# Performance work log

Hardware: AMD Instinct MI355X
Metric: run time of the kernel (lower is better)

Reference implementation:

```python
import jax, jax.numpy as jnp
import numpy as np

D_MODEL = 1024
NUM_HEADS = 16
D_K = D_MODEL // NUM_HEADS


def setup_inputs() -> dict:
    key = jax.random.key(0)
    ks = jax.random.split(key, 5)
    sd = np.sqrt(2.0 / (D_MODEL + D_MODEL))
    x = jax.random.normal(ks[0], (2, 2048, D_MODEL), dtype=jnp.float32)
    # weights stored as [out_features, in_features] like torch Linear
    w_q = jax.random.normal(ks[1], (D_MODEL, D_MODEL), dtype=jnp.float32) * (sd * sd)
    w_k = jax.random.normal(ks[2], (D_MODEL, D_MODEL), dtype=jnp.float32) * (sd * sd)
    w_v = jax.random.normal(ks[3], (D_MODEL, D_MODEL), dtype=jnp.float32) * (sd * sd)
    w_o = jax.random.normal(ks[4], (D_MODEL, D_MODEL), dtype=jnp.float32) * (sd * sd)
    return {"x": x, "w_q": w_q, "w_k": w_k, "w_v": w_v, "w_o": w_o}


def reference(x, w_q, w_k, w_v, w_o):
    B, S, D = x.shape
    H, Dk = NUM_HEADS, D_K
    # projections: x @ W.T
    q = (x @ w_q.T).reshape(B, S, H, Dk).transpose(0, 2, 1, 3)  # [B,H,S,Dk]
    k = (x @ w_k.T).reshape(B, S, H, Dk).transpose(0, 2, 1, 3)
    v = (x @ w_v.T).reshape(B, S, H, Dk).transpose(0, 2, 1, 3)
    scale = 1.0 / np.sqrt(Dk).astype(np.float32)
    scores = jnp.einsum('bhqd,bhkd->bhqk', q, k) * scale  # [B,H,S,S]
    causal = jnp.tril(jnp.ones((S, S), dtype=bool))
    scores = jnp.where(causal, scores, -jnp.inf)
    weights = jax.nn.softmax(scores, axis=-1)
    attn = jnp.einsum('bhqk,bhkd->bhqd', weights, v)  # [B,H,S,Dk]
    attn = attn.transpose(0, 2, 1, 3).reshape(B, S, D)
    return attn @ w_o.T
```

## Files before the change

### kernel.cpp

```cpp
#include <hip/hip_runtime.h>

typedef __attribute__((ext_vector_type(8))) short short8;
typedef __attribute__((ext_vector_type(4))) float f32x4;
typedef __attribute__((ext_vector_type(16))) float f32x16;
typedef __attribute__((ext_vector_type(2))) unsigned int u32x2;

#define DM 1024
#define SL 2048
#define NH 16
#define DKH 64
#define NB 2

__device__ __forceinline__ unsigned short f2bf(float f) {
    union { float f; unsigned int u; } a; a.f = f;
    unsigned int r = a.u + 0x7FFFu + ((a.u >> 16) & 1u);
    return (unsigned short)(r >> 16);
}

__device__ __forceinline__ void gl_lds16(const void* g, void* l) {
    __builtin_amdgcn_global_load_lds(
        (__attribute__((address_space(1))) void*)(g),
        (__attribute__((address_space(3))) void*)(l), 16, 0, 0);
}

__device__ __forceinline__ unsigned int cvtpk_bf16(float lo, float hi) {
    unsigned int r;
    asm("v_cvt_pk_bf16_f32 %0, %1, %2" : "=v"(r) : "v"(lo), "v"(hi));
    return r;
}

__device__ __forceinline__ void pl32swap(unsigned int &a, unsigned int &b) {
    u32x2 r = __builtin_amdgcn_permlane32_swap(a, b, false, false);
    a = r[0]; b = r[1];
}
__device__ __forceinline__ void pl32swapf(float &a, float &b) {
    unsigned int ua = __float_as_uint(a), ub = __float_as_uint(b);
    pl32swap(ua, ub);
    a = __uint_as_float(ua); b = __uint_as_float(ub);
}

__global__ __launch_bounds__(256) void convert_kernel(
    const float* __restrict__ x,  const float* __restrict__ wq,
    const float* __restrict__ wk, const float* __restrict__ wv,
    const float* __restrict__ wo,
    unsigned short* __restrict__ xb,  unsigned short* __restrict__ wqb,
    unsigned short* __restrict__ wkb, unsigned short* __restrict__ wvb,
    unsigned short* __restrict__ wob)
{
    const int NX = NB * SL * DM;
    const int NW = DM * DM;
    int t4 = (blockIdx.x * 256 + threadIdx.x) * 4;
    const float* src; unsigned short* dst; int off; float scale = 1.0f;
    if (t4 < NX)              { src = x;  dst = xb;  off = t4; }
    else if (t4 < NX + NW)    { src = wq; dst = wqb; off = t4 - NX; scale = 0.125f * 1.44269504088896f; }
    else if (t4 < NX + 2*NW)  { src = wk; dst = wkb; off = t4 - NX - NW; }
    else if (t4 < NX + 3*NW)  { src = wv; dst = wvb; off = t4 - NX - 2*NW; }
    else                      { src = wo; dst = wob; off = t4 - NX - 3*NW; }
    float4 v = *(const float4*)(src + off);
    unsigned long long p =
        (unsigned long long)f2bf(v.x * scale)
      | ((unsigned long long)f2bf(v.y * scale) << 16)
      | ((unsigned long long)f2bf(v.z * scale) << 32)
      | ((unsigned long long)f2bf(v.w * scale) << 48);
    *(unsigned long long*)(dst + off) = p;
}

__global__ __launch_bounds__(256) void gemm_bt(
    const unsigned short* __restrict__ A,
    const unsigned short* __restrict__ Bw,
    unsigned short* __restrict__ oq, unsigned short* __restrict__ ok,
    unsigned short* __restrict__ ov)
{
    __shared__ __align__(16) unsigned short As[128 * 64];
    __shared__ __align__(16) unsigned short Bs[128 * 64];
    const int tid  = threadIdx.x;
    const int lane = tid & 63;
    const int wave = tid >> 6;
    const int wm = (wave >> 1) * 64, wn = (wave & 1) * 64;
    const int bx = blockIdx.x, by = blockIdx.y;
    const int c    = lane & 15;
    const int kg16 = (lane >> 4) * 16;
    const int swz  = (c & 7) << 4;

    f32x4 acc[4][4];
    #pragma unroll
    for (int i = 0; i < 4; i++)
        #pragma unroll
        for (int j = 0; j < 4; j++) acc[i][j] = (f32x4){0.f, 0.f, 0.f, 0.f};

    const char* Ab = (const char*)A  + by * 128 * (DM * 2);
    const char* Bb = (const char*)Bw + bx * 128 * (DM * 2);

    for (int k0 = 0; k0 < DM; k0 += 64) {
        #pragma unroll
        for (int i = 0; i < 4; i++) {
            int o  = i * 4096 + tid * 16;
            int r  = o >> 7;
            int cb = o & 127;
            int src = r * (DM * 2) + k0 * 2 + (cb ^ ((r & 7) << 4));
            gl_lds16(Ab + src, (char*)As + o);
            gl_lds16(Bb + src, (char*)Bs + o);
        }
        __syncthreads();
        #pragma unroll
        for (int kk = 0; kk < 2; kk++) {
            short8 a[4], bfr[4];
            #pragma unroll
            for (int mi = 0; mi < 4; mi++)
                a[mi] = *(const short8*)((const char*)As
                        + (wm + mi * 16 + c) * 128 + ((kk * 64 + kg16) ^ swz));
            #pragma unroll
            for (int ni = 0; ni < 4; ni++)
                bfr[ni] = *(const short8*)((const char*)Bs
                        + (wn + ni * 16 + c) * 128 + ((kk * 64 + kg16) ^ swz));
            #pragma unroll
            for (int mi = 0; mi < 4; mi++)
                #pragma unroll
                for (int ni = 0; ni < 4; ni++)
                    acc[mi][ni] = __builtin_amdgcn_mfma_f32_16x16x32_bf16(
                        a[mi], bfr[ni], acc[mi][ni], 0, 0, 0);
        }
        __syncthreads();
    }

    const int r4 = (lane >> 4) * 4;
    const int mat = (bx * 128) >> 10;
    unsigned short* outb = (mat == 0) ? oq : (mat == 1) ? ok : ov;
    const int nb = bx * 128 - (mat << 10);
    #pragma unroll
    for (int mi = 0; mi < 4; mi++) {
        int m_g = by * 128 + wm + mi * 16 + r4;
        int b_  = m_g >> 11, s_ = m_g & 2047;
        #pragma unroll
        for (int ni = 0; ni < 4; ni++) {
            int n_l = nb + wn + ni * 16 + c;
            int h = n_l >> 6, dk = n_l & 63;
            #pragma unroll
            for (int j = 0; j < 4; j++)
                outb[((b_ * NH + h) * SL + (s_ + j)) * DKH + dk] = f2bf(acc[mi][ni][j]);
        }
    }
}

__global__ __launch_bounds__(256) void gemm_o(
    const unsigned short* __restrict__ A,
    const unsigned short* __restrict__ Bw,
    float* __restrict__ of)
{
    __shared__ __align__(16) unsigned short As[64 * 64];
    __shared__ __align__(16) unsigned short Bs[128 * 64];
    const int tid  = threadIdx.x;
    const int lane = tid & 63;
    const int wave = tid >> 6;
    const int wm = (wave >> 1) * 32, wn = (wave & 1) * 64;
    const int bx = blockIdx.x, by = blockIdx.y;
    const int c    = lane & 15;
    const int kg16 = (lane >> 4) * 16;
    const int swz  = (c & 7) << 4;

    f32x4 acc[2][4];
    #pragma unroll
    for (int i = 0; i < 2; i++)
        #pragma unroll
        for (int j = 0; j < 4; j++) acc[i][j] = (f32x4){0.f, 0.f, 0.f, 0.f};

    const char* Ab = (const char*)A  + by * 64  * (DM * 2);
    const char* Bb = (const char*)Bw + bx * 128 * (DM * 2);

    for (int k0 = 0; k0 < DM; k0 += 64) {
        #pragma unroll
        for (int i = 0; i < 2; i++) {
            int o  = i * 4096 + tid * 16;
            int r  = o >> 7, cb = o & 127;
            int src = r * (DM * 2) + k0 * 2 + (cb ^ ((r & 7) << 4));
            gl_lds16(Ab + src, (char*)As + o);
        }
        #pragma unroll
        for (int i = 0; i < 4; i++) {
            int o  = i * 4096 + tid * 16;
            int r  = o >> 7, cb = o & 127;
            int src = r * (DM * 2) + k0 * 2 + (cb ^ ((r & 7) << 4));
            gl_lds16(Bb + src, (char*)Bs + o);
        }
        __syncthreads();
        #pragma unroll
        for (int kk = 0; kk < 2; kk++) {
            short8 a[2], bfr[4];
            #pragma unroll
            for (int mi = 0; mi < 2; mi++)
                a[mi] = *(const short8*)((const char*)As
                        + (wm + mi * 16 + c) * 128 + ((kk * 64 + kg16) ^ swz));
            #pragma unroll
            for (int ni = 0; ni < 4; ni++)
                bfr[ni] = *(const short8*)((const char*)Bs
                        + (wn + ni * 16 + c) * 128 + ((kk * 64 + kg16) ^ swz));
            #pragma unroll
            for (int mi = 0; mi < 2; mi++)
                #pragma unroll
                for (int ni = 0; ni < 4; ni++)
                    acc[mi][ni] = __builtin_amdgcn_mfma_f32_16x16x32_bf16(
                        a[mi], bfr[ni], acc[mi][ni], 0, 0, 0);
        }
        __syncthreads();
    }

    const int r4 = (lane >> 4) * 4;
    #pragma unroll
    for (int mi = 0; mi < 2; mi++) {
        int m_g = by * 64 + wm + mi * 16 + r4;
        #pragma unroll
        for (int ni = 0; ni < 4; ni++) {
            int n_g = bx * 128 + wn + ni * 16 + c;
            #pragma unroll
            for (int j = 0; j < 4; j++)
                of[(m_g + j) * DM + n_g] = acc[mi][ni][j];
        }
    }
}

__global__ __launch_bounds__(128) void attn_kernel(
    const unsigned short* __restrict__ Q,
    const unsigned short* __restrict__ K,
    const unsigned short* __restrict__ V,
    unsigned short* __restrict__ O,
    unsigned short* __restrict__ partO,
    float* __restrict__ ml)
{
    __shared__ __align__(16) unsigned short Kl[2][64 * 64];
    __shared__ __align__(16) unsigned short Vt[2][8 * 64 * 8];
    const int tid = threadIdx.x, lane = tid & 63, wave = tid >> 6;
    const int ln31 = lane & 31, hi = lane >> 5;
    const int item = blockIdx.x >> 5;
    const int bh   = blockIdx.x & 31;
    int qt, cch, t0, ntc;
    if (item < 16)      { qt = 16 + item;              cch = 0; t0 = 0;  ntc = 16; }
    else if (item < 32) { int j = item - 16; qt = 31 - j; cch = 1; t0 = 16; ntc = 16 - j; }
    else                { int j = item - 32; qt = 15 - j; cch = 0; t0 = 0;  ntc = 16 - j; }
    const int b = bh >> 4, h = bh & 15;
    const int bhi = b * NH + h;
    const unsigned short* Qg = Q + bhi * (SL * DKH);
    const unsigned short* Kg = K + bhi * (SL * DKH);
    const unsigned short* Vg = V + bhi * (SL * DKH);
    const int qw = qt * 64 + wave * 32;
    const int vd0 = (tid & 31) * 2, c0 = tid >> 5;

    short8 qf[4];
    #pragma unroll
    for (int ks = 0; ks < 4; ks++)
        qf[ks] = *(const short8*)&Qg[(qw + ln31) * DKH + ks * 16 + hi * 8];

    f32x16 OT0, OT1;
    #pragma unroll
    for (int r = 0; r < 16; r++) { OT0[r] = 0.f; OT1[r] = 0.f; }
    float mrun = -1e30f, ls = 0.f;

    unsigned int vreg[16];

    {
        const size_t kvb = (size_t)t0 * 64;
        #pragma unroll
        for (int i = 0; i < 4; i++) {
            int s = i * 128 + tid;
            int kv = s >> 3;
            int k8 = (s & 7) ^ (kv & 7);
            gl_lds16((const char*)Kg + (kvb + kv) * 128 + k8 * 16,
                     (char*)&Kl[0][0] + s * 16);
        }
        #pragma unroll
        for (int c2 = 0; c2 < 2; c2++)
            #pragma unroll
            for (int i = 0; i < 8; i++)
                vreg[c2 * 8 + i] = *(const unsigned int*)&Vg[(kvb + (c0 + 4 * c2) * 8 + i) * DKH + vd0];
    }

    for (int tt = 0; tt < ntc; ++tt) {
        const int t = t0 + tt;
        const int buf = tt & 1;
        const int kv0 = t * 64;
        #pragma unroll
        for (int c2 = 0; c2 < 2; c2++) {
            int chunk = c0 + 4 * c2;
            short8 sa, sb;
            #pragma unroll
            for (int i = 0; i < 8; i++) {
                unsigned int pr = vreg[c2 * 8 + i];
                sa[i] = (short)(pr & 0xFFFFu);
                sb[i] = (short)(pr >> 16);
            }
            *(short8*)&Vt[buf][(chunk * 64 + vd0) * 8]     = sa;
            *(short8*)&Vt[buf][(chunk * 64 + vd0 + 1) * 8] = sb;
        }
        __syncthreads();

        if (tt + 1 < ntc) {
            const size_t kv1 = (size_t)(t + 1) * 64;
            #pragma unroll
            for (int i = 0; i < 4; i++) {
                int s = i * 128 + tid;
                int kv = s >> 3;
                int k8 = (s & 7) ^ (kv & 7);
                gl_lds16((const char*)Kg + (kv1 + kv) * 128 + k8 * 16,
                         (char*)&Kl[buf ^ 1][0] + s * 16);
            }
            #pragma unroll
            for (int c2 = 0; c2 < 2; c2++)
                #pragma unroll
                for (int i = 0; i < 8; i++)
                    vreg[c2 * 8 + i] = *(const unsigned int*)&Vg[(kv1 + (c0 + 4 * c2) * 8 + i) * DKH + vd0];
        }

        const char* kb = (const char*)&Kl[buf][0];
        const unsigned short* vb = &Vt[buf][0];

        f32x16 S0, S1;
        #pragma unroll
        for (int r = 0; r < 16; r++) { S0[r] = 0.f; S1[r] = 0.f; }
        __builtin_amdgcn_s_setprio(1);
        #pragma unroll
        for (int ks = 0; ks < 4; ks++) {
            int ko = (ks * 32 + hi * 16) ^ ((ln31 & 7) << 4);
            short8 ka0 = *(const short8*)(kb + ln31 * 128 + ko);
            short8 ka1 = *(const short8*)(kb + (32 + ln31) * 128 + ko);
            S0 = __builtin_amdgcn_mfma_f32_32x32x16_bf16(ka0, qf[ks], S0, 0, 0, 0);
            S1 = __builtin_amdgcn_mfma_f32_32x32x16_bf16(ka1, qf[ks], S1, 0, 0, 0);
        }
        __builtin_amdgcn_s_setprio(0);

        if (t == qt) {
            const int qrel0 = qw + ln31 - kv0 - 4 * hi;
            const int qrel1 = qrel0 - 32;
            #pragma unroll
            for (int r = 0; r < 16; r++) {
                const int ro = (r & 3) + 8 * (r >> 2);
                if (ro > qrel0) S0[r] = -1e30f;
                if (ro > qrel1) S1[r] = -1e30f;
            }
        }

        float mx = fmaxf(S0[0], S1[0]);
        #pragma unroll
        for (int r = 1; r < 16; r++) mx = fmaxf(mx, fmaxf(S0[r], S1[r]));
        float ma = mx, mb = mx;
        pl32swapf(ma, mb);
        float rm = fmaxf(ma, mb);

        if (__any(rm > mrun + 8.f)) {
            float nm = fmaxf(mrun, rm);
            float corr = __builtin_amdgcn_exp2f(mrun - nm);
            mrun = nm; ls *= corr;
            #pragma unroll
            for (int r = 0; r < 16; r++) { OT0[r] *= corr; OT1[r] *= corr; }
        }

        float psum = 0.f;
        #pragma unroll
        for (int r = 0; r < 16; r++) {
            S0[r] = __builtin_amdgcn_exp2f(S0[r] - mrun); psum += S0[r];
            S1[r] = __builtin_amdgcn_exp2f(S1[r] - mrun); psum += S1[r];
        }
        ls += psum;

        short8 pf[4];
        {
            unsigned int wa, wb, wc, wd;
            wa = cvtpk_bf16(S0[0], S0[1]);   wb = cvtpk_bf16(S0[4], S0[5]);
            pl32swap(wa, wb);
            wc = cvtpk_bf16(S0[2], S0[3]);   wd = cvtpk_bf16(S0[6], S0[7]);
            pl32swap(wc, wd);
            union { unsigned int u[4]; short8 s; } w0 = {{wa, wc, wb, wd}};
            pf[0] = w0.s;

            wa = cvtpk_bf16(S0[8], S0[9]);   wb = cvtpk_bf16(S0[12], S0[13]);
            pl32swap(wa, wb);
            wc = cvtpk_bf16(S0[10], S0[11]); wd = cvtpk_bf16(S0[14], S0[15]);
            pl32swap(wc, wd);
            union { unsigned int u[4]; short8 s; } w1 = {{wa, wc, wb, wd}};
            pf[1] = w1.s;

            wa = cvtpk_bf16(S1[0], S1[1]);   wb = cvtpk_bf16(S1[4], S1[5]);
            pl32swap(wa, wb);
            wc = cvtpk_bf16(S1[2], S1[3]);   wd = cvtpk_bf16(S1[6], S1[7]);
            pl32swap(wc, wd);
            union { unsigned int u[4]; short8 s; } w2 = {{wa, wc, wb, wd}};
            pf[2] = w2.s;

            wa = cvtpk_bf16(S1[8], S1[9]);   wb = cvtpk_bf16(S1[12], S1[13]);
            pl32swap(wa, wb);
            wc = cvtpk_bf16(S1[10], S1[11]); wd = cvtpk_bf16(S1[14], S1[15]);
            pl32swap(wc, wd);
            union { unsigned int u[4]; short8 s; } w3 = {{wa, wc, wb, wd}};
            pf[3] = w3.s;
        }

        __builtin_amdgcn_s_setprio(1);
        #pragma unroll
        for (int ks2 = 0; ks2 < 4; ks2++) {
            int slot = (ks2 * 2 + hi) * 64;
            short8 va0 = *(const short8*)&vb[(slot + ln31) * 8];
            short8 va1 = *(const short8*)&vb[(slot + 32 + ln31) * 8];
            OT0 = __builtin_amdgcn_mfma_f32_32x32x16_bf16(va0, pf[ks2], OT0, 0, 0, 0);
            OT1 = __builtin_amdgcn_mfma_f32_32x32x16_bf16(va1, pf[ks2], OT1, 0, 0, 0);
        }
        __builtin_amdgcn_s_setprio(0);
    }

    float la = ls, lb = ls;
    pl32swapf(la, lb);
    const float lrow = la + lb;
    const int qrow_l = wave * 32 + ln31;
    if (qt >= 16) {
        const int rec = (bh * 16 + (qt - 16)) * 2 + cch;
        unsigned short* po = partO + (size_t)rec * 4096;
        if (hi == 0) {
            ml[(rec * 64 + qrow_l) * 2]     = mrun;
            ml[(rec * 64 + qrow_l) * 2 + 1] = lrow;
        }
        #pragma unroll
        for (int r = 0; r < 16; r++) {
            const int d0 = (r & 3) + 8 * (r >> 2) + 4 * hi;
            po[qrow_l * 64 + d0]      = f2bf(OT0[r]);
            po[qrow_l * 64 + 32 + d0] = f2bf(OT1[r]);
        }
    } else {
        float inv = 1.0f / lrow;
        const int qrow = qw + ln31;
        const size_t base = (size_t)(b * SL + qrow) * DM + h * DKH;
        #pragma unroll
        for (int r = 0; r < 16; r++) {
            const int d0 = (r & 3) + 8 * (r >> 2) + 4 * hi;
            O[base + d0]      = f2bf(OT0[r] * inv);
            O[base + 32 + d0] = f2bf(OT1[r] * inv);
        }
    }
}

__global__ __launch_bounds__(256) void combine_kernel(
    const unsigned short* __restrict__ partO,
    const float* __restrict__ ml,
    unsigned short* __restrict__ O)
{
    const int gi = blockIdx.x * 8 + (threadIdx.x >> 5);
    const int ln = threadIdx.x & 31;
    const int bh = gi >> 10, rem = gi & 1023;
    const int qtl = rem >> 6, row = rem & 63;
    const int qt = 16 + qtl;
    const int rec0 = (bh * 16 + qtl) * 2;
    const float m0 = ml[(rec0 * 64 + row) * 2];
    const float l0 = ml[(rec0 * 64 + row) * 2 + 1];
    const float m1 = ml[((rec0 + 1) * 64 + row) * 2];
    const float l1 = ml[((rec0 + 1) * 64 + row) * 2 + 1];
    const float M  = fmaxf(m0, m1);
    const float w0 = exp2f(m0 - M), w1 = exp2f(m1 - M);
    const float inv = 1.0f / (w0 * l0 + w1 * l1);
    const unsigned int u0 = *(const unsigned int*)&partO[(size_t)rec0 * 4096 + row * 64 + ln * 2];
    const unsigned int u1 = *(const unsigned int*)&partO[(size_t)(rec0 + 1) * 4096 + row * 64 + ln * 2];
    const float a0 = __uint_as_float(u0 << 16);
    const float b0 = __uint_as_float(u0 & 0xFFFF0000u);
    const float a1 = __uint_as_float(u1 << 16);
    const float b1 = __uint_as_float(u1 & 0xFFFF0000u);
    const float oa = (a0 * w0 + a1 * w1) * inv;
    const float ob = (b0 * w0 + b1 * w1) * inv;
    const unsigned int pack = (unsigned int)f2bf(oa) | ((unsigned int)f2bf(ob) << 16);
    const int b = bh >> 4, h = bh & 15;
    const size_t base = (size_t)(b * SL + qt * 64 + row) * DM + h * DKH;
    *(unsigned int*)&O[base + ln * 2] = pack;
}

extern "C" void kernel_launch(void* const* d_in, const int* in_sizes, int n_in,
                              void* d_out, int out_size, void* d_ws, size_t ws_size,
                              hipStream_t stream)
{
    const float* x  = (const float*)d_in[0];
    const float* wq = (const float*)d_in[1];
    const float* wk = (const float*)d_in[2];
    const float* wv = (const float*)d_in[3];
    const float* wo = (const float*)d_in[4];
    char* ws = (char*)d_ws;
    unsigned short* xb  = (unsigned short*)(ws);
    unsigned short* wqb = (unsigned short*)(ws + (8ll  << 20));
    unsigned short* wkb = (unsigned short*)(ws + (10ll << 20));
    unsigned short* wvb = (unsigned short*)(ws + (12ll << 20));
    unsigned short* wob = (unsigned short*)(ws + (14ll << 20));
    unsigned short* Qb  = (unsigned short*)(ws + (16ll << 20));
    unsigned short* Kb  = (unsigned short*)(ws + (24ll << 20));
    unsigned short* Vb  = (unsigned short*)(ws + (32ll << 20));
    unsigned short* Abf = (unsigned short*)(ws + (40ll << 20));
    unsigned short* partO = (unsigned short*)(ws);
    float*          mlbuf = (float*)(ws + (8ll << 20));
    float* out = (float*)d_out;

    convert_kernel<<<dim3(8192), dim3(256), 0, stream>>>(
        x, wq, wk, wv, wo, xb, wqb, wkb, wvb, wob);

    gemm_bt<<<dim3(24, 32), dim3(256), 0, stream>>>(xb, wqb, Qb, Kb, Vb);

    attn_kernel<<<dim3(1536), dim3(128), 0, stream>>>(Qb, Kb, Vb, Abf, partO, mlbuf);
    combine_kernel<<<dim3(4096), dim3(256), 0, stream>>>(partO, mlbuf, Abf);

    gemm_o<<<dim3(8, 64), dim3(256), 0, stream>>>(Abf, wob, out);
}
```

Before: 104.8 us.

## Use 128-row query tiles with four waves sharing each K/V tile

The attention kernel now runs 256-thread blocks covering 128 query rows (four waves), so each K/V tile staged in LDS serves twice as many queries. The work split is rebuilt: query tiles 8-15 are split into two KV chunks that are merged by the combine kernel, and tiles 0-7 run unsplit. Waves whose rows lie entirely before a KV tile skip its compute but still join the barriers. The aim is to halve K/V global and LDS staging traffic per query. In exchange there are half as many blocks, more causal-mask waste on diagonal tiles, and some waves sit idle, which may hurt load balance.

```diff
diff --git a/kernel.cpp b/kernel.cpp
--- a/kernel.cpp
+++ b/kernel.cpp
@@ -218,7 +218,7 @@
     }
 }
 
-__global__ __launch_bounds__(128) void attn_kernel(
+__global__ __launch_bounds__(256) void attn_kernel(
     const unsigned short* __restrict__ Q,
     const unsigned short* __restrict__ K,
     const unsigned short* __restrict__ V,
@@ -230,18 +230,17 @@
     __shared__ __align__(16) unsigned short Vt[2][8 * 64 * 8];
     const int tid = threadIdx.x, lane = tid & 63, wave = tid >> 6;
     const int ln31 = lane & 31, hi = lane >> 5;
-    const int item = blockIdx.x >> 5;
-    const int bh   = blockIdx.x & 31;
-    int qt, cch, t0, ntc;
-    if (item < 16)      { qt = 16 + item;              cch = 0; t0 = 0;  ntc = 16; }
-    else if (item < 32) { int j = item - 16; qt = 31 - j; cch = 1; t0 = 16; ntc = 16 - j; }
-    else                { int j = item - 32; qt = 15 - j; cch = 0; t0 = 0;  ntc = 16 - j; }
+    const int w  = blockIdx.x >> 5;
+    const int bh = blockIdx.x & 31;
+    int p, cch, t0, ntc;
+    if (w < 16) { p = 15 - (w >> 1); cch = w & 1; ntc = p + 1; t0 = cch ? (p + 1) : 0; }
+    else        { p = 23 - w; cch = 0; t0 = 0; ntc = 2 * p + 2; }
     const int b = bh >> 4, h = bh & 15;
     const int bhi = b * NH + h;
     const unsigned short* Qg = Q + bhi * (SL * DKH);
     const unsigned short* Kg = K + bhi * (SL * DKH);
     const unsigned short* Vg = V + bhi * (SL * DKH);
-    const int qw = qt * 64 + wave * 32;
+    const int qw = p * 128 + wave * 32;
     const int vd0 = (tid & 31) * 2, c0 = tid >> 5;
 
     short8 qf[4];
@@ -254,60 +253,56 @@
     for (int r = 0; r < 16; r++) { OT0[r] = 0.f; OT1[r] = 0.f; }
     float mrun = -1e30f, ls = 0.f;
 
-    unsigned int vreg[16];
+    unsigned int vreg[8];
 
     {
         const size_t kvb = (size_t)t0 * 64;
         #pragma unroll
-        for (int i = 0; i < 4; i++) {
-            int s = i * 128 + tid;
+        for (int i = 0; i < 2; i++) {
+            int s = i * 256 + tid;
             int kv = s >> 3;
             int k8 = (s & 7) ^ (kv & 7);
             gl_lds16((const char*)Kg + (kvb + kv) * 128 + k8 * 16,
                      (char*)&Kl[0][0] + s * 16);
         }
         #pragma unroll
-        for (int c2 = 0; c2 < 2; c2++)
-            #pragma unroll
-            for (int i = 0; i < 8; i++)
-                vreg[c2 * 8 + i] = *(const unsigned int*)&Vg[(kvb + (c0 + 4 * c2) * 8 + i) * DKH + vd0];
+        for (int i = 0; i < 8; i++)
+            vreg[i] = *(const unsigned int*)&Vg[(kvb + c0 * 8 + i) * DKH + vd0];
     }
 
     for (int tt = 0; tt < ntc; ++tt) {
         const int t = t0 + tt;
         const int buf = tt & 1;
         const int kv0 = t * 64;
-        #pragma unroll
-        for (int c2 = 0; c2 < 2; c2++) {
-            int chunk = c0 + 4 * c2;
+        {
             short8 sa, sb;
             #pragma unroll
             for (int i = 0; i < 8; i++) {
-                unsigned int pr = vreg[c2 * 8 + i];
+                unsigned int pr = vreg[i];
                 sa[i] = (short)(pr & 0xFFFFu);
                 sb[i] = (short)(pr >> 16);
             }
-            *(short8*)&Vt[buf][(chunk * 64 + vd0) * 8]     = sa;
-            *(short8*)&Vt[buf][(chunk * 64 + vd0 + 1) * 8] = sb;
+            *(short8*)&Vt[buf][(c0 * 64 + vd0) * 8]     = sa;
+            *(short8*)&Vt[buf][(c0 * 64 + vd0 + 1) * 8] = sb;
         }
         __syncthreads();
 
         if (tt + 1 < ntc) {
             const size_t kv1 = (size_t)(t + 1) * 64;
             #pragma unroll
-            for (int i = 0; i < 4; i++) {
-                int s = i * 128 + tid;
+            for (int i = 0; i < 2; i++) {
+                int s = i * 256 + tid;
                 int kv = s >> 3;
                 int k8 = (s & 7) ^ (kv & 7);
                 gl_lds16((const char*)Kg + (kv1 + kv) * 128 + k8 * 16,
                          (char*)&Kl[buf ^ 1][0] + s * 16);
             }
             #pragma unroll
-            for (int c2 = 0; c2 < 2; c2++)
-                #pragma unroll
-                for (int i = 0; i < 8; i++)
-                    vreg[c2 * 8 + i] = *(const unsigned int*)&Vg[(kv1 + (c0 + 4 * c2) * 8 + i) * DKH + vd0];
-        }
+            for (int i = 0; i < 8; i++)
+                vreg[i] = *(const unsigned int*)&Vg[(kv1 + c0 * 8 + i) * DKH + vd0];
+        }
+
+        if (kv0 > qw + 31) continue;
 
         const char* kb = (const char*)&Kl[buf][0];
         const unsigned short* vb = &Vt[buf][0];
@@ -326,7 +321,7 @@
         }
         __builtin_amdgcn_s_setprio(0);
 
-        if (t == qt) {
+        if (kv0 + 63 > qw) {
             const int qrel0 = qw + ln31 - kv0 - 4 * hi;
             const int qrel1 = qrel0 - 32;
             #pragma unroll
@@ -408,12 +403,12 @@
     pl32swapf(la, lb);
     const float lrow = la + lb;
     const int qrow_l = wave * 32 + ln31;
-    if (qt >= 16) {
-        const int rec = (bh * 16 + (qt - 16)) * 2 + cch;
-        unsigned short* po = partO + (size_t)rec * 4096;
+    if (w < 16) {
+        const int rec = (bh * 8 + (p - 8)) * 2 + cch;
+        unsigned short* po = partO + (size_t)rec * 8192;
         if (hi == 0) {
-            ml[(rec * 64 + qrow_l) * 2]     = mrun;
-            ml[(rec * 64 + qrow_l) * 2 + 1] = lrow;
+            ml[(rec * 128 + qrow_l) * 2]     = mrun;
+            ml[(rec * 128 + qrow_l) * 2 + 1] = lrow;
         }
         #pragma unroll
         for (int r = 0; r < 16; r++) {
@@ -423,7 +418,7 @@
         }
     } else {
         float inv = 1.0f / lrow;
-        const int qrow = qw + ln31;
+        const int qrow = p * 128 + qrow_l;
         const size_t base = (size_t)(b * SL + qrow) * DM + h * DKH;
         #pragma unroll
         for (int r = 0; r < 16; r++) {
@@ -442,18 +437,18 @@
     const int gi = blockIdx.x * 8 + (threadIdx.x >> 5);
     const int ln = threadIdx.x & 31;
     const int bh = gi >> 10, rem = gi & 1023;
-    const int qtl = rem >> 6, row = rem & 63;
-    const int qt = 16 + qtl;
-    const int rec0 = (bh * 16 + qtl) * 2;
-    const float m0 = ml[(rec0 * 64 + row) * 2];
-    const float l0 = ml[(rec0 * 64 + row) * 2 + 1];
-    const float m1 = ml[((rec0 + 1) * 64 + row) * 2];
-    const float l1 = ml[((rec0 + 1) * 64 + row) * 2 + 1];
+    const int pi = rem >> 7, row = rem & 127;
+    const int p = 8 + pi;
+    const int rec0 = (bh * 8 + pi) * 2;
+    const float m0 = ml[(rec0 * 128 + row) * 2];
+    const float l0 = ml[(rec0 * 128 + row) * 2 + 1];
+    const float m1 = ml[((rec0 + 1) * 128 + row) * 2];
+    const float l1 = ml[((rec0 + 1) * 128 + row) * 2 + 1];
     const float M  = fmaxf(m0, m1);
     const float w0 = exp2f(m0 - M), w1 = exp2f(m1 - M);
     const float inv = 1.0f / (w0 * l0 + w1 * l1);
-    const unsigned int u0 = *(const unsigned int*)&partO[(size_t)rec0 * 4096 + row * 64 + ln * 2];
-    const unsigned int u1 = *(const unsigned int*)&partO[(size_t)(rec0 + 1) * 4096 + row * 64 + ln * 2];
+    const unsigned int u0 = *(const unsigned int*)&partO[(size_t)rec0 * 8192 + row * 64 + ln * 2];
+    const unsigned int u1 = *(const unsigned int*)&partO[(size_t)(rec0 + 1) * 8192 + row * 64 + ln * 2];
     const float a0 = __uint_as_float(u0 << 16);
     const float b0 = __uint_as_float(u0 & 0xFFFF0000u);
     const float a1 = __uint_as_float(u1 << 16);
@@ -462,7 +457,7 @@
     const float ob = (b0 * w0 + b1 * w1) * inv;
     const unsigned int pack = (unsigned int)f2bf(oa) | ((unsigned int)f2bf(ob) << 16);
     const int b = bh >> 4, h = bh & 15;
-    const size_t base = (size_t)(b * SL + qt * 64 + row) * DM + h * DKH;
+    const size_t base = (size_t)(b * SL + p * 128 + row) * DM + h * DKH;
     *(unsigned int*)&O[base + ln * 2] = pack;
 }
 
@@ -494,7 +489,7 @@
 
     gemm_bt<<<dim3(24, 32), dim3(256), 0, stream>>>(xb, wqb, Qb, Kb, Vb);
 
-    attn_kernel<<<dim3(1536), dim3(128), 0, stream>>>(Qb, Kb, Vb, Abf, partO, mlbuf);
+    attn_kernel<<<dim3(768), dim3(256), 0, stream>>>(Qb, Kb, Vb, Abf, partO, mlbuf);
     combine_kernel<<<dim3(4096), dim3(256), 0, stream>>>(partO, mlbuf, Abf);
 
     gemm_o<<<dim3(8, 64), dim3(256), 0, stream>>>(Abf, wob, out);
```

Measured after the change: 111.8 us. 1.07x slower.

## Halve attention KV tile to 32 and skip fully masked tiles per wave

Applied to the files above, without the earlier changes.

Reduces the KV tile from 64 to 32 rows, halving the shared-memory buffers and per-thread V staging registers, and doubles the number of loop iterations. Each wave now skips score and PV work for tiles lying entirely above its causal diagonal, and applies the mask to any tile that crosses the diagonal. The intent is to cut wasted MFMA and exp work on masked diagonal regions and to lower LDS and register pressure. In exchange it doubles the barrier and load-issue overhead per KV row, and each MFMA sequence is shorter, which gives less latency hiding.

```diff
diff --git a/kernel.cpp b/kernel.cpp
--- a/kernel.cpp
+++ b/kernel.cpp
@@ -226,16 +226,16 @@
     unsigned short* __restrict__ partO,
     float* __restrict__ ml)
 {
-    __shared__ __align__(16) unsigned short Kl[2][64 * 64];
-    __shared__ __align__(16) unsigned short Vt[2][8 * 64 * 8];
+    __shared__ __align__(16) unsigned short Kl[2][32 * 64];
+    __shared__ __align__(16) unsigned short Vt[2][4 * 64 * 8];
     const int tid = threadIdx.x, lane = tid & 63, wave = tid >> 6;
     const int ln31 = lane & 31, hi = lane >> 5;
     const int item = blockIdx.x >> 5;
     const int bh   = blockIdx.x & 31;
     int qt, cch, t0, ntc;
-    if (item < 16)      { qt = 16 + item;              cch = 0; t0 = 0;  ntc = 16; }
-    else if (item < 32) { int j = item - 16; qt = 31 - j; cch = 1; t0 = 16; ntc = 16 - j; }
-    else                { int j = item - 32; qt = 15 - j; cch = 0; t0 = 0;  ntc = 16 - j; }
+    if (item < 16)      { qt = 16 + item;              cch = 0; t0 = 0;  ntc = 32; }
+    else if (item < 32) { int j = item - 16; qt = 31 - j; cch = 1; t0 = 32; ntc = 32 - 2 * j; }
+    else                { int j = item - 32; qt = 15 - j; cch = 0; t0 = 0;  ntc = 32 - 2 * j; }
     const int b = bh >> 4, h = bh & 15;
     const int bhi = b * NH + h;
     const unsigned short* Qg = Q + bhi * (SL * DKH);
@@ -254,12 +254,12 @@
     for (int r = 0; r < 16; r++) { OT0[r] = 0.f; OT1[r] = 0.f; }
     float mrun = -1e30f, ls = 0.f;
 
-    unsigned int vreg[16];
+    unsigned int vreg[8];
 
     {
-        const size_t kvb = (size_t)t0 * 64;
-        #pragma unroll
-        for (int i = 0; i < 4; i++) {
+        const size_t kvb = (size_t)t0 * 32;
+        #pragma unroll
+        for (int i = 0; i < 2; i++) {
             int s = i * 128 + tid;
             int kv = s >> 3;
             int k8 = (s & 7) ^ (kv & 7);
@@ -267,35 +267,31 @@
                      (char*)&Kl[0][0] + s * 16);
         }
         #pragma unroll
-        for (int c2 = 0; c2 < 2; c2++)
-            #pragma unroll
-            for (int i = 0; i < 8; i++)
-                vreg[c2 * 8 + i] = *(const unsigned int*)&Vg[(kvb + (c0 + 4 * c2) * 8 + i) * DKH + vd0];
+        for (int i = 0; i < 8; i++)
+            vreg[i] = *(const unsigned int*)&Vg[(kvb + c0 * 8 + i) * DKH + vd0];
     }
 
     for (int tt = 0; tt < ntc; ++tt) {
         const int t = t0 + tt;
         const int buf = tt & 1;
-        const int kv0 = t * 64;
-        #pragma unroll
-        for (int c2 = 0; c2 < 2; c2++) {
-            int chunk = c0 + 4 * c2;
+        const int kv0 = t * 32;
+        {
             short8 sa, sb;
             #pragma unroll
             for (int i = 0; i < 8; i++) {
-                unsigned int pr = vreg[c2 * 8 + i];
+                unsigned int pr = vreg[i];
                 sa[i] = (short)(pr & 0xFFFFu);
                 sb[i] = (short)(pr >> 16);
             }
-            *(short8*)&Vt[buf][(chunk * 64 + vd0) * 8]     = sa;
-            *(short8*)&Vt[buf][(chunk * 64 + vd0 + 1) * 8] = sb;
+            *(short8*)&Vt[buf][(c0 * 64 + vd0) * 8]     = sa;
+            *(short8*)&Vt[buf][(c0 * 64 + vd0 + 1) * 8] = sb;
         }
         __syncthreads();
 
         if (tt + 1 < ntc) {
-            const size_t kv1 = (size_t)(t + 1) * 64;
-            #pragma unroll
-            for (int i = 0; i < 4; i++) {
+            const size_t kv1 = (size_t)(t + 1) * 32;
+            #pragma unroll
+            for (int i = 0; i < 2; i++) {
                 int s = i * 128 + tid;
                 int kv = s >> 3;
                 int k8 = (s & 7) ^ (kv & 7);
@@ -303,43 +299,39 @@
                          (char*)&Kl[buf ^ 1][0] + s * 16);
             }
             #pragma unroll
-            for (int c2 = 0; c2 < 2; c2++)
-                #pragma unroll
-                for (int i = 0; i < 8; i++)
-                    vreg[c2 * 8 + i] = *(const unsigned int*)&Vg[(kv1 + (c0 + 4 * c2) * 8 + i) * DKH + vd0];
-        }
+            for (int i = 0; i < 8; i++)
+                vreg[i] = *(const unsigned int*)&Vg[(kv1 + c0 * 8 + i) * DKH + vd0];
+        }
+
+        if (kv0 > qw + 31) continue;
 
         const char* kb = (const char*)&Kl[buf][0];
         const unsigned short* vb = &Vt[buf][0];
 
-        f32x16 S0, S1;
-        #pragma unroll
-        for (int r = 0; r < 16; r++) { S0[r] = 0.f; S1[r] = 0.f; }
+        f32x16 S0;
+        #pragma unroll
+        for (int r = 0; r < 16; r++) S0[r] = 0.f;
         __builtin_amdgcn_s_setprio(1);
         #pragma unroll
         for (int ks = 0; ks < 4; ks++) {
             int ko = (ks * 32 + hi * 16) ^ ((ln31 & 7) << 4);
             short8 ka0 = *(const short8*)(kb + ln31 * 128 + ko);
-            short8 ka1 = *(const short8*)(kb + (32 + ln31) * 128 + ko);
             S0 = __builtin_amdgcn_mfma_f32_32x32x16_bf16(ka0, qf[ks], S0, 0, 0, 0);
-            S1 = __builtin_amdgcn_mfma_f32_32x32x16_bf16(ka1, qf[ks], S1, 0, 0, 0);
         }
         __builtin_amdgcn_s_setprio(0);
 
-        if (t == qt) {
+        if (kv0 + 31 > qw) {
             const int qrel0 = qw + ln31 - kv0 - 4 * hi;
-            const int qrel1 = qrel0 - 32;
             #pragma unroll
             for (int r = 0; r < 16; r++) {
                 const int ro = (r & 3) + 8 * (r >> 2);
                 if (ro > qrel0) S0[r] = -1e30f;
-                if (ro > qrel1) S1[r] = -1e30f;
             }
         }
 
-        float mx = fmaxf(S0[0], S1[0]);
-        #pragma unroll
-        for (int r = 1; r < 16; r++) mx = fmaxf(mx, fmaxf(S0[r], S1[r]));
+        float mx = S0[0];
+        #pragma unroll
+        for (int r = 1; r < 16; r++) mx = fmaxf(mx, S0[r]);
         float ma = mx, mb = mx;
         pl32swapf(ma, mb);
         float rm = fmaxf(ma, mb);
@@ -356,11 +348,10 @@
         #pragma unroll
         for (int r = 0; r < 16; r++) {
             S0[r] = __builtin_amdgcn_exp2f(S0[r] - mrun); psum += S0[r];
-            S1[r] = __builtin_amdgcn_exp2f(S1[r] - mrun); psum += S1[r];
         }
         ls += psum;
 
-        short8 pf[4];
+        short8 pf[2];
         {
             unsigned int wa, wb, wc, wd;
             wa = cvtpk_bf16(S0[0], S0[1]);   wb = cvtpk_bf16(S0[4], S0[5]);
@@ -376,25 +367,11 @@
             pl32swap(wc, wd);
             union { unsigned int u[4]; short8 s; } w1 = {{wa, wc, wb, wd}};
             pf[1] = w1.s;
-
-            wa = cvtpk_bf16(S1[0], S1[1]);   wb = cvtpk_bf16(S1[4], S1[5]);
-            pl32swap(wa, wb);
-            wc = cvtpk_bf16(S1[2], S1[3]);   wd = cvtpk_bf16(S1[6], S1[7]);
-            pl32swap(wc, wd);
-            union { unsigned int u[4]; short8 s; } w2 = {{wa, wc, wb, wd}};
-            pf[2] = w2.s;
-
-            wa = cvtpk_bf16(S1[8], S1[9]);   wb = cvtpk_bf16(S1[12], S1[13]);
-            pl32swap(wa, wb);
-            wc = cvtpk_bf16(S1[10], S1[11]); wd = cvtpk_bf16(S1[14], S1[15]);
-            pl32swap(wc, wd);
-            union { unsigned int u[4]; short8 s; } w3 = {{wa, wc, wb, wd}};
-            pf[3] = w3.s;
         }
 
         __builtin_amdgcn_s_setprio(1);
         #pragma unroll
-        for (int ks2 = 0; ks2 < 4; ks2++) {
+        for (int ks2 = 0; ks2 < 2; ks2++) {
             int slot = (ks2 * 2 + hi) * 64;
             short8 va0 = *(const short8*)&vb[(slot + ln31) * 8];
             short8 va1 = *(const short8*)&vb[(slot + 32 + ln31) * 8];
```

After: 113.5 us. 1.08x slower.
